# Kernel tuning notes

Hardware: AMD Instinct MI355X
Metric: run time of the kernel (lower is better)

The kernel has to match this reference:

```python
import jax, jax.numpy as jnp
import numpy as np

D = 1024
EXPAND = 2
DI = EXPAND * D
K = 4           # d_conv
C = 64          # chunk_size
ALPHA = 0.9     # memory decay
B, S = 2, 8192
EPS = 1e-5


def setup_inputs() -> dict:
    key = jax.random.key(0)
    ks = jax.random.split(key, 10)
    s = 0.02
    return {
        "x": jax.random.normal(ks[0], (B, S, D), dtype=jnp.float32),
        "norm_w": jnp.ones((D,), dtype=jnp.float32),
        "w_up": jax.random.normal(ks[1], (D, DI), dtype=jnp.float32) * s,
        "w_gate": jax.random.normal(ks[2], (D, DI), dtype=jnp.float32) * s,
        "w_down": jax.random.normal(ks[3], (DI, D), dtype=jnp.float32) * s,
        "conv_w": jax.random.normal(ks[4], (K, 1, DI), dtype=jnp.float32) * s,  # WIO depthwise
        "conv_b": jnp.zeros((DI,), dtype=jnp.float32),
        "wq": jax.random.normal(ks[5], (D, D), dtype=jnp.float32) * s,
        "wk": jax.random.normal(ks[6], (D, D), dtype=jnp.float32) * s,
        "wv": jax.random.normal(ks[7], (D, D), dtype=jnp.float32) * s,
        "wo": jax.random.normal(ks[8], (D, D), dtype=jnp.float32) * s,
    }


def _rmsnorm(x, w):
    ms = jnp.mean(jnp.square(x.astype(jnp.float32)), axis=-1, keepdims=True)
    return (x * jax.lax.rsqrt(ms + EPS).astype(x.dtype)) * w


def _causal_depthwise_conv(u, conv_w, conv_b):
    # u: [B,S,DI]; depthwise causal conv over S, then SiLU
    y = jax.lax.conv_general_dilated(
        u, conv_w,
        window_strides=(1,), padding=[(K - 1, 0)],
        dimension_numbers=("NWC", "WIO", "NWC"),
        feature_group_count=DI)
    return jax.nn.silu(y + conv_b)


def _hebbian_memory(h, wq, wk, wv, wo):
    # chunked linear-attention style Hebbian memory
    b, s, d = h.shape
    n = s // C
    scale = d ** -0.5
    q = (h @ wq).reshape(b, n, C, d) * scale
    k = (h @ wk).reshape(b, n, C, d)
    v = (h @ wv).reshape(b, n, C, d)
    mask = jnp.tril(jnp.ones((C, C), dtype=h.dtype))  # inclusive causal within chunk

    def step(M, qkv):
        qc, kc, vc = qkv  # [b,C,d]
        inter = jnp.einsum("bcd,bde->bce", qc, M)
        attn = jnp.einsum("bcd,bed->bce", qc, kc) * mask
        intra = jnp.einsum("bce,bed->bcd", attn, vc)
        M_new = ALPHA * M + jnp.einsum("bcd,bce->bde", kc, vc)
        return M_new, inter + intra

    M0 = jnp.zeros((b, d, d), dtype=h.dtype)
    qkv = (jnp.swapaxes(q, 0, 1), jnp.swapaxes(k, 0, 1), jnp.swapaxes(v, 0, 1))
    _, o = jax.lax.scan(step, M0, qkv)        # [n,b,C,d]
    o = jnp.swapaxes(o, 0, 1).reshape(b, s, d)
    return o @ wo


def reference(x, norm_w, w_up, w_gate, w_down, conv_w, conv_b, wq, wk, wv, wo):
    normed = _rmsnorm(x, norm_w)
    val = _causal_depthwise_conv(normed @ w_up, conv_w, conv_b)   # [B,S,DI]
    gate = jax.nn.silu(normed @ w_gate)
    out = (gate * val) @ w_down                                   # [B,S,D]
    out = _hebbian_memory(out, wq, wk, wv, wo)
    return x + out
```

## Files before the change

### kernel.cpp

```cpp
#include <hip/hip_runtime.h>
#include <cstdint>
#include <cstddef>

#define SS 8192
#define DD 1024
#define DI2 2048
#define NR 16384

#define LOG2_09 (-0.152003093445050f)
#define LAMBDA16 0.185302018885184f

typedef __attribute__((ext_vector_type(4))) float f32x4;
typedef __attribute__((ext_vector_type(8))) __bf16 bf16x8;

union U16 { uint4 u; bf16x8 b; };

static __device__ __forceinline__ f32x4 MFMA(uint4 a, uint4 b, f32x4 c) {
  U16 ua, ub; ua.u = a; ub.u = b;
  return __builtin_amdgcn_mfma_f32_16x16x32_bf16(ua.b, ub.b, c, 0, 0, 0);
}

static __device__ __forceinline__ unsigned short f2bf(float f) {
  union { float f; unsigned u; } v; v.f = f;
  return (unsigned short)((v.u + 0x7FFFu + ((v.u >> 16) & 1u)) >> 16);
}
static __device__ __forceinline__ float bf2f(unsigned b) {
  union { unsigned u; float f; } v; v.u = b << 16; return v.f;
}
static __device__ __forceinline__ void unpack8(uint4 u, float* f) {
  f[0] = bf2f(u.x & 0xFFFFu); f[1] = bf2f(u.x >> 16);
  f[2] = bf2f(u.y & 0xFFFFu); f[3] = bf2f(u.y >> 16);
  f[4] = bf2f(u.z & 0xFFFFu); f[5] = bf2f(u.z >> 16);
  f[6] = bf2f(u.w & 0xFFFFu); f[7] = bf2f(u.w >> 16);
}
static __device__ __forceinline__ uint4 scale8(uint4 u, float w) {
  float f[8]; unpack8(u, f);
  uint4 o;
  o.x = (unsigned)f2bf(f[0] * w) | ((unsigned)f2bf(f[1] * w) << 16);
  o.y = (unsigned)f2bf(f[2] * w) | ((unsigned)f2bf(f[3] * w) << 16);
  o.z = (unsigned)f2bf(f[4] * w) | ((unsigned)f2bf(f[5] * w) << 16);
  o.w = (unsigned)f2bf(f[6] * w) | ((unsigned)f2bf(f[7] * w) << 16);
  return o;
}

static __device__ __forceinline__ void glds16(const unsigned short* g, char* l) {
  __builtin_amdgcn_global_load_lds(
      (const __attribute__((address_space(1))) unsigned int*)g,
      (__attribute__((address_space(3))) unsigned int*)l, 16, 0, 0);
}

static __device__ __forceinline__ int swz64(int row, int kb) { return ((row << 6) | kb) ^ ((row & 7) << 4); }

__global__ __launch_bounds__(256)
void transpose_cast(const float* __restrict__ in, unsigned short* __restrict__ out, int R, int Cc) {
  __shared__ float tile[32][33];
  const int r0 = blockIdx.y * 32, c0 = blockIdx.x * 32;
  const int tx = threadIdx.x, ty = threadIdx.y;
#pragma unroll
  for (int i = 0; i < 4; i++)
    tile[ty + i * 8][tx] = in[(size_t)(r0 + ty + i * 8) * Cc + c0 + tx];
  __syncthreads();
#pragma unroll
  for (int i = 0; i < 4; i++)
    out[(size_t)(c0 + ty + i * 8) * R + r0 + tx] = f2bf(tile[tx][ty + i * 8]);
}

__global__ __launch_bounds__(256)
void rmsnorm_kernel(const float* __restrict__ x, const float* __restrict__ w,
                    unsigned short* __restrict__ out) {
  const int row = blockIdx.x, t = threadIdx.x;
  const float4 v = ((const float4*)(x + (size_t)row * DD))[t];
  float ss = v.x * v.x + v.y * v.y + v.z * v.z + v.w * v.w;
  __shared__ float sred[256];
  sred[t] = ss;
  __syncthreads();
  for (int o = 128; o > 0; o >>= 1) {
    if (t < o) sred[t] += sred[t + o];
    __syncthreads();
  }
  const float rr = rsqrtf(sred[0] * (1.0f / (float)DD) + 1e-5f);
  const float4 wv = ((const float4*)w)[t];
  uint2 pk;
  pk.x = (unsigned)f2bf(v.x * rr * wv.x) | ((unsigned)f2bf(v.y * rr * wv.y) << 16);
  pk.y = (unsigned)f2bf(v.z * rr * wv.z) | ((unsigned)f2bf(v.w * rr * wv.w) << 16);
  *(uint2*)(out + (size_t)row * DD + t * 4) = pk;
}

enum { EP_BF16 = 0, EP_BF16_BOTH = 1, EP_BF16_T = 2, EP_F32_RES = 3 };

template <int MODE>
__global__ __launch_bounds__(512, 2)
void gemm256(const unsigned short* __restrict__ A, const unsigned short* __restrict__ Bt,
             unsigned short* __restrict__ Cb, unsigned short* __restrict__ Ct,
             float* __restrict__ Cf, const float* __restrict__ resid,
             int M, int N, int K, float scale) {
  __shared__ char sLds[131072];
  const int t = threadIdx.x, lane = t & 63, wid = t >> 6;
  const int wr = wid >> 2, wc = wid & 3;
  const int l15 = lane & 15, lh = lane >> 4;
  const int mblocks = M >> 8;
  const int msl = mblocks >> 3;
  const int xcd = (int)blockIdx.x & 7, loc = (int)blockIdx.x >> 3;
  const int m0 = (xcd * msl + (loc % msl)) << 8;
  const int n0 = (loc / msl) << 8;
  const int srow = wid * 16 + (lane >> 2);
  const int scol = ((lane & 3) << 3) ^ (((srow >> 1) & 3) << 3);
  const unsigned short* pA0 = A + (size_t)(m0 + srow) * K + scol;
  const unsigned short* pA1 = pA0 + (size_t)128 * K;
  const unsigned short* pB0 = Bt + (size_t)(n0 + srow) * K + scol;
  const unsigned short* pB1 = pB0 + (size_t)128 * K;
  const int ldsW = wid * 1024;
  int offA[8], offB[4];
#pragma unroll
  for (int mf = 0; mf < 8; mf++) {
    const int r = wr * 128 + mf * 16 + l15;
    offA[mf] = r * 64 + ((lh * 16) ^ (((r >> 1) & 3) << 4));
  }
#pragma unroll
  for (int nf = 0; nf < 4; nf++) {
    const int r = wc * 64 + nf * 16 + l15;
    offB[nf] = r * 64 + ((lh * 16) ^ (((r >> 1) & 3) << 4));
  }
  const int NT = K >> 5;
#define BUFA(tt) (sLds + ((tt) & 3) * 32768)
#define BUFB(tt) (sLds + ((tt) & 3) * 32768 + 16384)
#define STAGEA(tt) do { const int _k = (tt) * 32; \
    glds16(pA0 + _k, BUFA(tt) + ldsW); \
    glds16(pA1 + _k, BUFA(tt) + 8192 + ldsW); } while (0)
#define STAGEB(tt) do { const int _k = (tt) * 32; \
    glds16(pB0 + _k, BUFB(tt) + ldsW); \
    glds16(pB1 + _k, BUFB(tt) + 8192 + ldsW); } while (0)
  STAGEA(0); STAGEB(0); STAGEA(1); STAGEB(1); STAGEA(2); STAGEB(2);
  asm volatile("s_waitcnt vmcnt(8)" ::: "memory");
  __builtin_amdgcn_s_barrier();
  f32x4 acc[8][4] = {};
  for (int kt = 0; kt < NT; ++kt) {
    const char* At  = BUFA(kt);
    const char* Bt_ = BUFB(kt);
    uint4 av[4], bv[4], av2[4];
#pragma unroll
    for (int i = 0; i < 4; i++) av[i] = *(const uint4*)(At + offA[i]);
#pragma unroll
    for (int i = 0; i < 4; i++) bv[i] = *(const uint4*)(Bt_ + offB[i]);
    if (kt + 3 < NT) STAGEA(kt + 3);
    asm volatile("s_waitcnt lgkmcnt(0)" ::: "memory");
    __builtin_amdgcn_sched_barrier(0);
    __builtin_amdgcn_s_setprio(1);
#pragma unroll
    for (int mf = 0; mf < 4; mf++)
#pragma unroll
      for (int nf = 0; nf < 4; nf++)
        acc[mf][nf] = MFMA(av[mf], bv[nf], acc[mf][nf]);
    __builtin_amdgcn_s_setprio(0);
    __builtin_amdgcn_s_barrier();
#pragma unroll
    for (int i = 0; i < 4; i++) av2[i] = *(const uint4*)(At + offA[4 + i]);
    if (kt + 3 < NT) STAGEB(kt + 3);
    asm volatile("s_waitcnt lgkmcnt(0)" ::: "memory");
    __builtin_amdgcn_sched_barrier(0);
    __builtin_amdgcn_s_setprio(1);
#pragma unroll
    for (int mf = 0; mf < 4; mf++)
#pragma unroll
      for (int nf = 0; nf < 4; nf++)
        acc[4 + mf][nf] = MFMA(av2[mf], bv[nf], acc[4 + mf][nf]);
    __builtin_amdgcn_s_setprio(0);
    if (kt < NT - 3)       { asm volatile("s_waitcnt vmcnt(8)" ::: "memory"); }
    else if (kt == NT - 3) { asm volatile("s_waitcnt vmcnt(4)" ::: "memory"); }
    else if (kt == NT - 2) { asm volatile("s_waitcnt vmcnt(0)" ::: "memory"); }
    __builtin_amdgcn_s_barrier();
  }
#undef STAGEA
#undef STAGEB
#undef BUFA
#undef BUFB
#pragma unroll
  for (int mf = 0; mf < 8; mf++) {
    const int r0 = m0 + wr * 128 + mf * 16 + lh * 4;
#pragma unroll
    for (int nf = 0; nf < 4; nf++) {
      const int c = n0 + wc * 64 + nf * 16 + l15;
      f32x4 v = acc[mf][nf] * scale;
      if constexpr (MODE == EP_F32_RES) {
#pragma unroll
        for (int jj = 0; jj < 4; jj++) {
          const size_t idx = (size_t)(r0 + jj) * N + c;
          Cf[idx] = v[jj] + resid[idx];
        }
      } else {
        if constexpr (MODE == EP_BF16 || MODE == EP_BF16_BOTH) {
#pragma unroll
          for (int jj = 0; jj < 4; jj++)
            Cb[(size_t)(r0 + jj) * N + c] = f2bf(v[jj]);
        }
        if constexpr (MODE == EP_BF16_BOTH || MODE == EP_BF16_T) {
          const int bb = r0 >> 13, s0 = r0 & (SS - 1);
          uint2 pk;
          pk.x = (unsigned)f2bf(v[0]) | ((unsigned)f2bf(v[1]) << 16);
          pk.y = (unsigned)f2bf(v[2]) | ((unsigned)f2bf(v[3]) << 16);
          *(uint2*)(Ct + ((size_t)bb * DD + c) * SS + s0) = pk;
        }
      }
    }
  }
}

__global__ __launch_bounds__(256)
void convgate_kernel(const unsigned short* __restrict__ ug, const float* __restrict__ cw,
                     const float* __restrict__ cb, unsigned short* __restrict__ hin) {
  const int r = blockIdx.x;
  const int c0 = threadIdx.x * 8;
  const int s = r & (SS - 1);
  float acc[8];
#pragma unroll
  for (int i = 0; i < 8; i++) acc[i] = cb[c0 + i];
  for (int tap = 0; tap < 4; tap++) {
    const int ds = s - 3 + tap;
    if (ds < 0) continue;
    uint4 uv = *(const uint4*)(ug + (size_t)(r - 3 + tap) * 4096 + c0);
    float u[8]; unpack8(uv, u);
#pragma unroll
    for (int i = 0; i < 8; i++) acc[i] += u[i] * cw[tap * DI2 + c0 + i];
  }
  uint4 gv = *(const uint4*)(ug + (size_t)r * 4096 + DI2 + c0);
  float gt[8]; unpack8(gv, gt);
  unsigned short o16[8];
#pragma unroll
  for (int i = 0; i < 8; i++) {
    const float val = acc[i] / (1.0f + __expf(-acc[i]));
    const float gg  = gt[i] / (1.0f + __expf(-gt[i]));
    o16[i] = f2bf(val * gg);
  }
  uint4 ov;
  ov.x = (unsigned)o16[0] | ((unsigned)o16[1] << 16);
  ov.y = (unsigned)o16[2] | ((unsigned)o16[3] << 16);
  ov.z = (unsigned)o16[4] | ((unsigned)o16[5] << 16);
  ov.w = (unsigned)o16[6] | ((unsigned)o16[7] << 16);
  *(uint4*)(hin + (size_t)r * DI2 + c0) = ov;
}

__global__ __launch_bounds__(256)
void state_gemm(const unsigned short* __restrict__ vt, const unsigned short* __restrict__ kt,
                unsigned short* __restrict__ Tb) {
  __shared__ char sA[8192];
  __shared__ char sB[8192];
  const int t = threadIdx.x, lane = t & 63, wid = t >> 6;
  const int wr = wid >> 1, wc = wid & 1;
  const int l15 = lane & 15, lh = lane >> 4;
  const int gb = blockIdx.z, b = gb >> 3, g = gb & 7;
  const int m0 = blockIdx.y * 128, n0 = blockIdx.x * 128;
  const int sr = t >> 2, skb = (t & 3) * 16;
  const size_t kofs = (size_t)g * 1024;
  const unsigned short* Ar0 = vt + (size_t)(b * DD + m0 + sr) * SS + kofs;
  const unsigned short* Ar1 = Ar0 + (size_t)64 * SS;
  const unsigned short* Br0 = kt + (size_t)(b * DD + n0 + sr) * SS + kofs;
  const unsigned short* Br1 = Br0 + (size_t)64 * SS;
  f32x4 acc[4][4] = {};
  for (int k0 = 0; k0 < 1024; k0 += 32) {
    const int ke = k0 + (t & 3) * 8;
    const float w = exp2f((float)(15 - (ke >> 6)) * LOG2_09);
    uint4 ra0 = scale8(*(const uint4*)(Ar0 + ke), w);
    uint4 ra1 = scale8(*(const uint4*)(Ar1 + ke), w);
    uint4 rb0 = *(const uint4*)(Br0 + ke);
    uint4 rb1 = *(const uint4*)(Br1 + ke);
    __syncthreads();
    *(uint4*)(sA + swz64(sr, skb)) = ra0;
    *(uint4*)(sA + swz64(sr + 64, skb)) = ra1;
    *(uint4*)(sB + swz64(sr, skb)) = rb0;
    *(uint4*)(sB + swz64(sr + 64, skb)) = rb1;
    __syncthreads();
    uint4 af[4], bfr[4];
#pragma unroll
    for (int i = 0; i < 4; i++) af[i]  = *(uint4*)(sA + swz64(wr * 64 + i * 16 + l15, lh * 16));
#pragma unroll
    for (int i = 0; i < 4; i++) bfr[i] = *(uint4*)(sB + swz64(wc * 64 + i * 16 + l15, lh * 16));
#pragma unroll
    for (int mf = 0; mf < 4; mf++)
#pragma unroll
      for (int nf = 0; nf < 4; nf++)
        acc[mf][nf] = MFMA(af[mf], bfr[nf], acc[mf][nf]);
  }
  unsigned short* Tg = Tb + ((size_t)gb << 20);
#pragma unroll
  for (int mf = 0; mf < 4; mf++) {
    const int r0 = m0 + wr * 64 + mf * 16 + lh * 4;
#pragma unroll
    for (int nf = 0; nf < 4; nf++) {
      const int c = n0 + wc * 64 + nf * 16 + l15;
#pragma unroll
      for (int jj = 0; jj < 4; jj++)
        Tg[(size_t)(r0 + jj) * 1024 + c] = f2bf(acc[mf][nf][jj]);
    }
  }
}

__global__ __launch_bounds__(256)
void prefix_kernel(unsigned short* __restrict__ Tb) {
  const int tid = blockIdx.x * 256 + threadIdx.x;
  const int b = tid >> 17, i = tid & 131071;
  unsigned short* p = Tb + (((size_t)b * 8) << 20) + (size_t)i * 8;
  float acc[8] = {};
  for (int g = 0; g < 8; g++) {
    unsigned short* pg = p + ((size_t)g << 20);
    uint4 tv = *(uint4*)pg;
    float tf_[8]; unpack8(tv, tf_);
    uint4 ov;
    ov.x = (unsigned)f2bf(acc[0]) | ((unsigned)f2bf(acc[1]) << 16);
    ov.y = (unsigned)f2bf(acc[2]) | ((unsigned)f2bf(acc[3]) << 16);
    ov.z = (unsigned)f2bf(acc[4]) | ((unsigned)f2bf(acc[5]) << 16);
    ov.w = (unsigned)f2bf(acc[6]) | ((unsigned)f2bf(acc[7]) << 16);
    *(uint4*)pg = ov;
#pragma unroll
    for (int e = 0; e < 8; e++) acc[e] = LAMBDA16 * acc[e] + tf_[e];
  }
}

__global__ __launch_bounds__(256)
void score_attn(const unsigned short* __restrict__ q, const unsigned short* __restrict__ k,
                unsigned short* __restrict__ sbuf) {
  __shared__ char sQ[4096];
  __shared__ char sK[4096];
  const int p = blockIdx.x, gb = blockIdx.y;
  int qt = (int)((sqrtf(8.0f * p + 1.0f) - 1.0f) * 0.5f);
  while ((qt + 1) * (qt + 2) / 2 <= p) qt++;
  while (qt * (qt + 1) / 2 > p) qt--;
  const int tb = p - qt * (qt + 1) / 2;
  const int b = gb >> 3, g = gb & 7;
  const int t = threadIdx.x, lane = t & 63, wid = t >> 6;
  const int l15 = lane & 15, lh = lane >> 4;
  const int srow = wid * 16 + (lane >> 2), scol = (lane & 3) * 8;
  const unsigned short* qg = q + (size_t)(b * SS + g * 1024 + qt * 64 + srow) * DD + scol;
  const unsigned short* kg = k + (size_t)(b * SS + g * 1024 + tb * 64 + srow) * DD + scol;
  char* lQ = sQ + wid * 1024;
  char* lK = sK + wid * 1024;
  f32x4 s[4] = {};
  for (int k0 = 0; k0 < DD; k0 += 32) {
    glds16(qg + k0, lQ);
    glds16(kg + k0, lK);
    __syncthreads();
    uint4 aq = *(uint4*)(sQ + (wid * 16 + l15) * 64 + lh * 16);
#pragma unroll
    for (int tf = 0; tf < 4; tf++) {
      uint4 bk = *(uint4*)(sK + (tf * 16 + l15) * 64 + lh * 16);
      s[tf] = MFMA(aq, bk, s[tf]);
    }
    __syncthreads();
  }
  const bool diag = (tb == qt);
  const float w = diag ? 1.0f : exp2f((float)(qt - 1 - tb) * LOG2_09);
  unsigned short* sb = sbuf + ((size_t)(gb * 16 + qt) * 64) * 1024 + tb * 64;
#pragma unroll
  for (int tf = 0; tf < 4; tf++)
#pragma unroll
    for (int jj = 0; jj < 4; jj++) {
      const int qr = wid * 16 + lh * 4 + jj;
      const int tc = tf * 16 + l15;
      float val = s[tf][jj] * w;
      if (diag && tc > qr) val = 0.0f;
      sb[(size_t)qr * 1024 + tc] = f2bf(val);
    }
}

__global__ __launch_bounds__(256)
void pv_attn(const unsigned short* __restrict__ sbuf, const unsigned short* __restrict__ vt,
             unsigned short* __restrict__ obuf) {
  __shared__ char sA[4096];
  __shared__ char sB[8192];
  const int et = blockIdx.x, qt = blockIdx.y, gb = blockIdx.z;
  const int b = gb >> 3, g = gb & 7;
  const int t = threadIdx.x, lane = t & 63, wid = t >> 6;
  const int l15 = lane & 15, lh = lane >> 4;
  const int srow = wid * 16 + (lane >> 2), scol = (lane & 3) * 8;
  const int e0 = et * 128;
  const unsigned short* Ag = sbuf + ((size_t)(gb * 16 + qt) * 64 + srow) * 1024 + scol;
  const unsigned short* Bg0 = vt + ((size_t)b * DD + e0 + srow) * SS + g * 1024 + scol;
  const unsigned short* Bg1 = Bg0 + (size_t)64 * SS;
  char* lA  = sA + wid * 1024;
  char* lB0 = sB + wid * 1024;
  char* lB1 = sB + 4096 + wid * 1024;
  const int tEnd = (qt + 1) * 64;
  f32x4 o[4][2] = {};
  for (int t0 = 0; t0 < tEnd; t0 += 32) {
    glds16(Ag + t0, lA);
    glds16(Bg0 + t0, lB0);
    glds16(Bg1 + t0, lB1);
    __syncthreads();
    uint4 af[4], vf[2];
#pragma unroll
    for (int mf = 0; mf < 4; mf++) af[mf] = *(uint4*)(sA + (mf * 16 + l15) * 64 + lh * 16);
#pragma unroll
    for (int nf = 0; nf < 2; nf++) vf[nf] = *(uint4*)(sB + (wid * 32 + nf * 16 + l15) * 64 + lh * 16);
#pragma unroll
    for (int mf = 0; mf < 4; mf++)
#pragma unroll
      for (int nf = 0; nf < 2; nf++)
        o[mf][nf] = MFMA(af[mf], vf[nf], o[mf][nf]);
    __syncthreads();
  }
  const size_t qrow0 = (size_t)b * SS + (size_t)g * 1024 + (size_t)qt * 64;
#pragma unroll
  for (int mf = 0; mf < 4; mf++)
#pragma unroll
    for (int nf = 0; nf < 2; nf++)
#pragma unroll
      for (int jj = 0; jj < 4; jj++)
        obuf[(qrow0 + mf * 16 + lh * 4 + jj) * DD + e0 + wid * 32 + nf * 16 + l15] =
            f2bf(o[mf][nf][jj]);
}

__global__ __launch_bounds__(256)
void cross_gemm(const unsigned short* __restrict__ q, const unsigned short* __restrict__ Minit,
                unsigned short* __restrict__ obuf) {
  __shared__ char sA[8192];
  __shared__ char sB[8192];
  const int t = threadIdx.x, lane = t & 63, wid = t >> 6;
  const int wr = wid >> 1, wc = wid & 1;
  const int l15 = lane & 15, lh = lane >> 4;
  const int gb = blockIdx.z, b = gb >> 3, g = gb & 7;
  const int m0 = blockIdx.y * 128, n0 = blockIdx.x * 128;
  const int srow = wid * 16 + (lane >> 2), scol = (lane & 3) * 8;
  const unsigned short* Ar0 = q + (size_t)(b * SS + g * 1024 + m0 + srow) * DD + scol;
  const unsigned short* Ar1 = Ar0 + (size_t)64 * DD;
  const unsigned short* Br0 = Minit + ((size_t)gb << 20) + (size_t)(n0 + srow) * 1024 + scol;
  const unsigned short* Br1 = Br0 + (size_t)64 * 1024;
  char* lA0 = sA + wid * 1024;
  char* lA1 = sA + 4096 + wid * 1024;
  char* lB0 = sB + wid * 1024;
  char* lB1 = sB + 4096 + wid * 1024;
  f32x4 acc[4][4] = {};
  for (int k0 = 0; k0 < 1024; k0 += 32) {
    glds16(Ar0 + k0, lA0);
    glds16(Ar1 + k0, lA1);
    glds16(Br0 + k0, lB0);
    glds16(Br1 + k0, lB1);
    __syncthreads();
    uint4 af[4], bfr[4];
#pragma unroll
    for (int i = 0; i < 4; i++) af[i]  = *(uint4*)(sA + (wr * 64 + i * 16 + l15) * 64 + lh * 16);
#pragma unroll
    for (int i = 0; i < 4; i++) bfr[i] = *(uint4*)(sB + (wc * 64 + i * 16 + l15) * 64 + lh * 16);
#pragma unroll
    for (int mf = 0; mf < 4; mf++)
#pragma unroll
      for (int nf = 0; nf < 4; nf++)
        acc[mf][nf] = MFMA(af[mf], bfr[nf], acc[mf][nf]);
    __syncthreads();
  }
#pragma unroll
  for (int mf = 0; mf < 4; mf++) {
    const int rl = m0 + wr * 64 + mf * 16 + lh * 4;
#pragma unroll
    for (int nf = 0; nf < 4; nf++) {
      const int c = n0 + wc * 64 + nf * 16 + l15;
#pragma unroll
      for (int jj = 0; jj < 4; jj++) {
        const int r = rl + jj;
        const float rs = exp2f((float)(r >> 6) * LOG2_09);
        const size_t idx = ((size_t)b * SS + (size_t)g * 1024 + r) * DD + c;
        obuf[idx] = f2bf(bf2f(obuf[idx]) + acc[mf][nf][jj] * rs);
      }
    }
  }
}

extern "C" void kernel_launch(void* const* d_in, const int* in_sizes, int n_in,
                              void* d_out, int out_size, void* d_ws, size_t ws_size,
                              hipStream_t stream) {
  (void)in_sizes; (void)n_in; (void)out_size;
  const float* x      = (const float*)d_in[0];
  const float* norm_w = (const float*)d_in[1];
  const float* w_up   = (const float*)d_in[2];
  const float* w_gate = (const float*)d_in[3];
  const float* w_down = (const float*)d_in[4];
  const float* conv_w = (const float*)d_in[5];
  const float* conv_b = (const float*)d_in[6];
  const float* wq     = (const float*)d_in[7];
  const float* wk     = (const float*)d_in[8];
  const float* wv     = (const float*)d_in[9];
  const float* wo     = (const float*)d_in[10];
  float* out = (float*)d_out;

  const size_t MB = 1ull << 20;
  if (ws_size < 212 * MB) return;
  char* base = (char*)d_ws;
  unsigned short* ug     = (unsigned short*)(base + 0);
  unsigned short* hbuf   = (unsigned short*)(base + 0);
  unsigned short* Tbuf   = (unsigned short*)(base + 0);
  unsigned short* qbuf   = (unsigned short*)(base + 32 * MB);
  unsigned short* kbuf   = (unsigned short*)(base + 64 * MB);
  unsigned short* ktbuf  = (unsigned short*)(base + 96 * MB);
  unsigned short* sbuf   = (unsigned short*)(base + 96 * MB);
  unsigned short* normed = (unsigned short*)(base + 128 * MB);
  unsigned short* hin    = (unsigned short*)(base + 128 * MB);
  unsigned short* vtbuf  = (unsigned short*)(base + 128 * MB);
  unsigned short* obuf   = (unsigned short*)(base + 160 * MB);
  unsigned short* wugt   = (unsigned short*)(base + 192 * MB);
  unsigned short* wdt    = (unsigned short*)(base + 200 * MB);
  unsigned short* wqt    = (unsigned short*)(base + 204 * MB);
  unsigned short* wkt    = (unsigned short*)(base + 206 * MB);
  unsigned short* wvt    = (unsigned short*)(base + 208 * MB);
  unsigned short* wot    = (unsigned short*)(base + 210 * MB);

  dim3 tb(32, 8);
  transpose_cast<<<dim3(DI2 / 32, DD / 32), tb, 0, stream>>>(w_up,   wugt,                    DD,  DI2);
  transpose_cast<<<dim3(DI2 / 32, DD / 32), tb, 0, stream>>>(w_gate, wugt + (size_t)DI2 * DD, DD,  DI2);
  transpose_cast<<<dim3(DD / 32, DI2 / 32), tb, 0, stream>>>(w_down, wdt, DI2, DD);
  transpose_cast<<<dim3(DD / 32, DD / 32),  tb, 0, stream>>>(wq, wqt, DD, DD);
  transpose_cast<<<dim3(DD / 32, DD / 32),  tb, 0, stream>>>(wk, wkt, DD, DD);
  transpose_cast<<<dim3(DD / 32, DD / 32),  tb, 0, stream>>>(wv, wvt, DD, DD);
  transpose_cast<<<dim3(DD / 32, DD / 32),  tb, 0, stream>>>(wo, wot, DD, DD);

  rmsnorm_kernel<<<NR, 256, 0, stream>>>(x, norm_w, normed);

  gemm256<EP_BF16><<<dim3((NR / 256) * (4096 / 256)), 512, 0, stream>>>(
      normed, wugt, ug, nullptr, nullptr, nullptr, NR, 4096, DD, 1.0f);

  convgate_kernel<<<NR, 256, 0, stream>>>(ug, conv_w, conv_b, hin);

  gemm256<EP_BF16><<<dim3((NR / 256) * (DD / 256)), 512, 0, stream>>>(
      hin, wdt, hbuf, nullptr, nullptr, nullptr, NR, DD, DI2, 1.0f);

  gemm256<EP_BF16><<<dim3((NR / 256) * (DD / 256)), 512, 0, stream>>>(
      hbuf, wqt, qbuf, nullptr, nullptr, nullptr, NR, DD, DD, 0.03125f);
  gemm256<EP_BF16_BOTH><<<dim3((NR / 256) * (DD / 256)), 512, 0, stream>>>(
      hbuf, wkt, kbuf, ktbuf, nullptr, nullptr, NR, DD, DD, 1.0f);
  gemm256<EP_BF16_T><<<dim3((NR / 256) * (DD / 256)), 512, 0, stream>>>(
      hbuf, wvt, nullptr, vtbuf, nullptr, nullptr, NR, DD, DD, 1.0f);

  state_gemm<<<dim3(8, 8, 16), 256, 0, stream>>>(vtbuf, ktbuf, Tbuf);
  score_attn<<<dim3(136, 16), 256, 0, stream>>>(qbuf, kbuf, sbuf);
  prefix_kernel<<<1024, 256, 0, stream>>>(Tbuf);
  pv_attn<<<dim3(8, 16, 16), 256, 0, stream>>>(sbuf, vtbuf, obuf);
  cross_gemm<<<dim3(8, 8, 16), 256, 0, stream>>>(qbuf, Tbuf, obuf);

  gemm256<EP_F32_RES><<<dim3((NR / 256) * (DD / 256)), 512, 0, stream>>>(
      obuf, wot, nullptr, nullptr, out, x, NR, DD, DD, 1.0f);
}
```

Measured before the change: 760.5 us.

## Route state and cross GEMMs through the pipelined 256-tile GEMM kernel

Removes the separate state_gemm and cross_gemm kernels and runs both through the gemm256 template with new epilogue modes, added lda/ldb strides and batched z-dimension offsets. The decay weighting that state_gemm applied to V on the fly moves into the K-transpose epilogue of the K projection GEMM. The 128x128 single-buffered tiles are replaced by the 256x256 four-stage global-to-LDS pipeline. Extra s_barrier calls are inserted after each staging step in the main loop, which adds synchronisation to every GEMM, and each state/cross launch now has only 256 blocks.

```diff
diff --git a/kernel.cpp b/kernel.cpp
--- a/kernel.cpp
+++ b/kernel.cpp
@@ -33,23 +33,12 @@
   f[4] = bf2f(u.z & 0xFFFFu); f[5] = bf2f(u.z >> 16);
   f[6] = bf2f(u.w & 0xFFFFu); f[7] = bf2f(u.w >> 16);
 }
-static __device__ __forceinline__ uint4 scale8(uint4 u, float w) {
-  float f[8]; unpack8(u, f);
-  uint4 o;
-  o.x = (unsigned)f2bf(f[0] * w) | ((unsigned)f2bf(f[1] * w) << 16);
-  o.y = (unsigned)f2bf(f[2] * w) | ((unsigned)f2bf(f[3] * w) << 16);
-  o.z = (unsigned)f2bf(f[4] * w) | ((unsigned)f2bf(f[5] * w) << 16);
-  o.w = (unsigned)f2bf(f[6] * w) | ((unsigned)f2bf(f[7] * w) << 16);
-  return o;
-}
 
 static __device__ __forceinline__ void glds16(const unsigned short* g, char* l) {
   __builtin_amdgcn_global_load_lds(
       (const __attribute__((address_space(1))) unsigned int*)g,
       (__attribute__((address_space(3))) unsigned int*)l, 16, 0, 0);
 }
-
-static __device__ __forceinline__ int swz64(int row, int kb) { return ((row << 6) | kb) ^ ((row & 7) << 4); }
 
 __global__ __launch_bounds__(256)
 void transpose_cast(const float* __restrict__ in, unsigned short* __restrict__ out, int R, int Cc) {
@@ -86,29 +75,49 @@
   *(uint2*)(out + (size_t)row * DD + t * 4) = pk;
 }
 
-enum { EP_BF16 = 0, EP_BF16_BOTH = 1, EP_BF16_T = 2, EP_F32_RES = 3 };
+enum { EP_BF16 = 0, EP_BF16_BOTH = 1, EP_BF16_T = 2, EP_F32_RES = 3, EP_STATE = 4, EP_CROSS = 5 };
 
 template <int MODE>
 __global__ __launch_bounds__(512, 2)
 void gemm256(const unsigned short* __restrict__ A, const unsigned short* __restrict__ Bt,
              unsigned short* __restrict__ Cb, unsigned short* __restrict__ Ct,
              float* __restrict__ Cf, const float* __restrict__ resid,
-             int M, int N, int K, float scale) {
+             int M, int N, int kLen, int lda, int ldb, float scale) {
   __shared__ char sLds[131072];
   const int t = threadIdx.x, lane = t & 63, wid = t >> 6;
   const int wr = wid >> 2, wc = wid & 3;
   const int l15 = lane & 15, lh = lane >> 4;
   const int mblocks = M >> 8;
-  const int msl = mblocks >> 3;
-  const int xcd = (int)blockIdx.x & 7, loc = (int)blockIdx.x >> 3;
-  const int m0 = (xcd * msl + (loc % msl)) << 8;
-  const int n0 = (loc / msl) << 8;
+  int m0, n0;
+  if ((mblocks & 7) == 0) {
+    const int msl = mblocks >> 3;
+    const int xcd = (int)blockIdx.x & 7, loc = (int)blockIdx.x >> 3;
+    m0 = (xcd * msl + (loc % msl)) << 8;
+    n0 = (loc / msl) << 8;
+  } else {
+    m0 = ((int)blockIdx.x % mblocks) << 8;
+    n0 = ((int)blockIdx.x / mblocks) << 8;
+  }
+  int zb = 0, zg = 0;
+  const unsigned short* Abase = A;
+  const unsigned short* Bbase = Bt;
+  if constexpr (MODE == EP_STATE || MODE == EP_CROSS) {
+    const int gb = blockIdx.z;
+    zb = gb >> 3; zg = gb & 7;
+    if constexpr (MODE == EP_STATE) {
+      Abase = A + (size_t)zb * DD * SS + (size_t)zg * 1024;
+      Bbase = Bt + (size_t)zb * DD * SS + (size_t)zg * 1024;
+    } else {
+      Abase = A + ((size_t)zb * SS + (size_t)zg * 1024) * (size_t)lda;
+      Bbase = Bt + ((size_t)blockIdx.z << 20);
+    }
+  }
   const int srow = wid * 16 + (lane >> 2);
   const int scol = ((lane & 3) << 3) ^ (((srow >> 1) & 3) << 3);
-  const unsigned short* pA0 = A + (size_t)(m0 + srow) * K + scol;
-  const unsigned short* pA1 = pA0 + (size_t)128 * K;
-  const unsigned short* pB0 = Bt + (size_t)(n0 + srow) * K + scol;
-  const unsigned short* pB1 = pB0 + (size_t)128 * K;
+  const unsigned short* pA0 = Abase + (size_t)(m0 + srow) * lda + scol;
+  const unsigned short* pA1 = pA0 + (size_t)128 * lda;
+  const unsigned short* pB0 = Bbase + (size_t)(n0 + srow) * ldb + scol;
+  const unsigned short* pB1 = pB0 + (size_t)128 * ldb;
   const int ldsW = wid * 1024;
   int offA[8], offB[4];
 #pragma unroll
@@ -121,7 +130,7 @@
     const int r = wc * 64 + nf * 16 + l15;
     offB[nf] = r * 64 + ((lh * 16) ^ (((r >> 1) & 3) << 4));
   }
-  const int NT = K >> 5;
+  const int NT = kLen >> 5;
 #define BUFA(tt) (sLds + ((tt) & 3) * 32768)
 #define BUFB(tt) (sLds + ((tt) & 3) * 32768 + 16384)
 #define STAGEA(tt) do { const int _k = (tt) * 32; \
@@ -143,6 +152,7 @@
 #pragma unroll
     for (int i = 0; i < 4; i++) bv[i] = *(const uint4*)(Bt_ + offB[i]);
     if (kt + 3 < NT) STAGEA(kt + 3);
+    __builtin_amdgcn_s_barrier();
     asm volatile("s_waitcnt lgkmcnt(0)" ::: "memory");
     __builtin_amdgcn_sched_barrier(0);
     __builtin_amdgcn_s_setprio(1);
@@ -156,6 +166,7 @@
 #pragma unroll
     for (int i = 0; i < 4; i++) av2[i] = *(const uint4*)(At + offA[4 + i]);
     if (kt + 3 < NT) STAGEB(kt + 3);
+    __builtin_amdgcn_s_barrier();
     asm volatile("s_waitcnt lgkmcnt(0)" ::: "memory");
     __builtin_amdgcn_sched_barrier(0);
     __builtin_amdgcn_s_setprio(1);
@@ -187,6 +198,18 @@
           const size_t idx = (size_t)(r0 + jj) * N + c;
           Cf[idx] = v[jj] + resid[idx];
         }
+      } else if constexpr (MODE == EP_STATE) {
+        unsigned short* Tg = Cb + ((size_t)blockIdx.z << 20);
+#pragma unroll
+        for (int jj = 0; jj < 4; jj++)
+          Tg[(size_t)(r0 + jj) * 1024 + c] = f2bf(v[jj]);
+      } else if constexpr (MODE == EP_CROSS) {
+        const float rs = exp2f((float)(r0 >> 6) * LOG2_09);
+#pragma unroll
+        for (int jj = 0; jj < 4; jj++) {
+          const size_t idx = ((size_t)zb * SS + (size_t)zg * 1024 + r0 + jj) * DD + c;
+          Cb[idx] = f2bf(bf2f(Cb[idx]) + v[jj] * rs);
+        }
       } else {
         if constexpr (MODE == EP_BF16 || MODE == EP_BF16_BOTH) {
 #pragma unroll
@@ -195,9 +218,12 @@
         }
         if constexpr (MODE == EP_BF16_BOTH || MODE == EP_BF16_T) {
           const int bb = r0 >> 13, s0 = r0 & (SS - 1);
+          float wt = 1.0f;
+          if constexpr (MODE == EP_BF16_BOTH)
+            wt = exp2f((float)(15 - ((s0 >> 6) & 15)) * LOG2_09);
           uint2 pk;
-          pk.x = (unsigned)f2bf(v[0]) | ((unsigned)f2bf(v[1]) << 16);
-          pk.y = (unsigned)f2bf(v[2]) | ((unsigned)f2bf(v[3]) << 16);
+          pk.x = (unsigned)f2bf(v[0] * wt) | ((unsigned)f2bf(v[1] * wt) << 16);
+          pk.y = (unsigned)f2bf(v[2] * wt) | ((unsigned)f2bf(v[3] * wt) << 16);
           *(uint2*)(Ct + ((size_t)bb * DD + c) * SS + s0) = pk;
         }
       }
@@ -237,61 +263,6 @@
   ov.z = (unsigned)o16[4] | ((unsigned)o16[5] << 16);
   ov.w = (unsigned)o16[6] | ((unsigned)o16[7] << 16);
   *(uint4*)(hin + (size_t)r * DI2 + c0) = ov;
-}
-
-__global__ __launch_bounds__(256)
-void state_gemm(const unsigned short* __restrict__ vt, const unsigned short* __restrict__ kt,
-                unsigned short* __restrict__ Tb) {
-  __shared__ char sA[8192];
-  __shared__ char sB[8192];
-  const int t = threadIdx.x, lane = t & 63, wid = t >> 6;
-  const int wr = wid >> 1, wc = wid & 1;
-  const int l15 = lane & 15, lh = lane >> 4;
-  const int gb = blockIdx.z, b = gb >> 3, g = gb & 7;
-  const int m0 = blockIdx.y * 128, n0 = blockIdx.x * 128;
-  const int sr = t >> 2, skb = (t & 3) * 16;
-  const size_t kofs = (size_t)g * 1024;
-  const unsigned short* Ar0 = vt + (size_t)(b * DD + m0 + sr) * SS + kofs;
-  const unsigned short* Ar1 = Ar0 + (size_t)64 * SS;
-  const unsigned short* Br0 = kt + (size_t)(b * DD + n0 + sr) * SS + kofs;
-  const unsigned short* Br1 = Br0 + (size_t)64 * SS;
-  f32x4 acc[4][4] = {};
-  for (int k0 = 0; k0 < 1024; k0 += 32) {
-    const int ke = k0 + (t & 3) * 8;
-    const float w = exp2f((float)(15 - (ke >> 6)) * LOG2_09);
-    uint4 ra0 = scale8(*(const uint4*)(Ar0 + ke), w);
-    uint4 ra1 = scale8(*(const uint4*)(Ar1 + ke), w);
-    uint4 rb0 = *(const uint4*)(Br0 + ke);
-    uint4 rb1 = *(const uint4*)(Br1 + ke);
-    __syncthreads();
-    *(uint4*)(sA + swz64(sr, skb)) = ra0;
-    *(uint4*)(sA + swz64(sr + 64, skb)) = ra1;
-    *(uint4*)(sB + swz64(sr, skb)) = rb0;
-    *(uint4*)(sB + swz64(sr + 64, skb)) = rb1;
-    __syncthreads();
-    uint4 af[4], bfr[4];
-#pragma unroll
-    for (int i = 0; i < 4; i++) af[i]  = *(uint4*)(sA + swz64(wr * 64 + i * 16 + l15, lh * 16));
-#pragma unroll
-    for (int i = 0; i < 4; i++) bfr[i] = *(uint4*)(sB + swz64(wc * 64 + i * 16 + l15, lh * 16));
-#pragma unroll
-    for (int mf = 0; mf < 4; mf++)
-#pragma unroll
-      for (int nf = 0; nf < 4; nf++)
-        acc[mf][nf] = MFMA(af[mf], bfr[nf], acc[mf][nf]);
-  }
-  unsigned short* Tg = Tb + ((size_t)gb << 20);
-#pragma unroll
-  for (int mf = 0; mf < 4; mf++) {
-    const int r0 = m0 + wr * 64 + mf * 16 + lh * 4;
-#pragma unroll
-    for (int nf = 0; nf < 4; nf++) {
-      const int c = n0 + wc * 64 + nf * 16 + l15;
-#pragma unroll
-      for (int jj = 0; jj < 4; jj++)
-        Tg[(size_t)(r0 + jj) * 1024 + c] = f2bf(acc[mf][nf][jj]);
-    }
-  }
 }
 
 __global__ __launch_bounds__(256)
@@ -408,61 +379,6 @@
             f2bf(o[mf][nf][jj]);
 }
 
-__global__ __launch_bounds__(256)
-void cross_gemm(const unsigned short* __restrict__ q, const unsigned short* __restrict__ Minit,
-                unsigned short* __restrict__ obuf) {
-  __shared__ char sA[8192];
-  __shared__ char sB[8192];
-  const int t = threadIdx.x, lane = t & 63, wid = t >> 6;
-  const int wr = wid >> 1, wc = wid & 1;
-  const int l15 = lane & 15, lh = lane >> 4;
-  const int gb = blockIdx.z, b = gb >> 3, g = gb & 7;
-  const int m0 = blockIdx.y * 128, n0 = blockIdx.x * 128;
-  const int srow = wid * 16 + (lane >> 2), scol = (lane & 3) * 8;
-  const unsigned short* Ar0 = q + (size_t)(b * SS + g * 1024 + m0 + srow) * DD + scol;
-  const unsigned short* Ar1 = Ar0 + (size_t)64 * DD;
-  const unsigned short* Br0 = Minit + ((size_t)gb << 20) + (size_t)(n0 + srow) * 1024 + scol;
-  const unsigned short* Br1 = Br0 + (size_t)64 * 1024;
-  char* lA0 = sA + wid * 1024;
-  char* lA1 = sA + 4096 + wid * 1024;
-  char* lB0 = sB + wid * 1024;
-  char* lB1 = sB + 4096 + wid * 1024;
-  f32x4 acc[4][4] = {};
-  for (int k0 = 0; k0 < 1024; k0 += 32) {
-    glds16(Ar0 + k0, lA0);
-    glds16(Ar1 + k0, lA1);
-    glds16(Br0 + k0, lB0);
-    glds16(Br1 + k0, lB1);
-    __syncthreads();
-    uint4 af[4], bfr[4];
-#pragma unroll
-    for (int i = 0; i < 4; i++) af[i]  = *(uint4*)(sA + (wr * 64 + i * 16 + l15) * 64 + lh * 16);
-#pragma unroll
-    for (int i = 0; i < 4; i++) bfr[i] = *(uint4*)(sB + (wc * 64 + i * 16 + l15) * 64 + lh * 16);
-#pragma unroll
-    for (int mf = 0; mf < 4; mf++)
-#pragma unroll
-      for (int nf = 0; nf < 4; nf++)
-        acc[mf][nf] = MFMA(af[mf], bfr[nf], acc[mf][nf]);
-    __syncthreads();
-  }
-#pragma unroll
-  for (int mf = 0; mf < 4; mf++) {
-    const int rl = m0 + wr * 64 + mf * 16 + lh * 4;
-#pragma unroll
-    for (int nf = 0; nf < 4; nf++) {
-      const int c = n0 + wc * 64 + nf * 16 + l15;
-#pragma unroll
-      for (int jj = 0; jj < 4; jj++) {
-        const int r = rl + jj;
-        const float rs = exp2f((float)(r >> 6) * LOG2_09);
-        const size_t idx = ((size_t)b * SS + (size_t)g * 1024 + r) * DD + c;
-        obuf[idx] = f2bf(bf2f(obuf[idx]) + acc[mf][nf][jj] * rs);
-      }
-    }
-  }
-}
-
 extern "C" void kernel_launch(void* const* d_in, const int* in_sizes, int n_in,
                               void* d_out, int out_size, void* d_ws, size_t ws_size,
                               hipStream_t stream) {
@@ -513,26 +429,28 @@
   rmsnorm_kernel<<<NR, 256, 0, stream>>>(x, norm_w, normed);
 
   gemm256<EP_BF16><<<dim3((NR / 256) * (4096 / 256)), 512, 0, stream>>>(
-      normed, wugt, ug, nullptr, nullptr, nullptr, NR, 4096, DD, 1.0f);
+      normed, wugt, ug, nullptr, nullptr, nullptr, NR, 4096, DD, DD, DD, 1.0f);
 
   convgate_kernel<<<NR, 256, 0, stream>>>(ug, conv_w, conv_b, hin);
 
   gemm256<EP_BF16><<<dim3((NR / 256) * (DD / 256)), 512, 0, stream>>>(
-      hin, wdt, hbuf, nullptr, nullptr, nullptr, NR, DD, DI2, 1.0f);
+      hin, wdt, hbuf, nullptr, nullptr, nullptr, NR, DD, DI2, DI2, DI2, 1.0f);
 
   gemm256<EP_BF16><<<dim3((NR / 256) * (DD / 256)), 512, 0, stream>>>(
-      hbuf, wqt, qbuf, nullptr, nullptr, nullptr, NR, DD, DD, 0.03125f);
+      hbuf, wqt, qbuf, nullptr, nullptr, nullptr, NR, DD, DD, DD, DD, 0.03125f);
   gemm256<EP_BF16_BOTH><<<dim3((NR / 256) * (DD / 256)), 512, 0, stream>>>(
-      hbuf, wkt, kbuf, ktbuf, nullptr, nullptr, NR, DD, DD, 1.0f);
+      hbuf, wkt, kbuf, ktbuf, nullptr, nullptr, NR, DD, DD, DD, DD, 1.0f);
   gemm256<EP_BF16_T><<<dim3((NR / 256) * (DD / 256)), 512, 0, stream>>>(
-      hbuf, wvt, nullptr, vtbuf, nullptr, nullptr, NR, DD, DD, 1.0f);
-
-  state_gemm<<<dim3(8, 8, 16), 256, 0, stream>>>(vtbuf, ktbuf, Tbuf);
+      hbuf, wvt, nullptr, vtbuf, nullptr, nullptr, NR, DD, DD, DD, DD, 1.0f);
+
+  gemm256<EP_STATE><<<dim3(16, 1, 16), 512, 0, stream>>>(
+      vtbuf, ktbuf, Tbuf, nullptr, nullptr, nullptr, 1024, 1024, 1024, SS, SS, 1.0f);
   score_attn<<<dim3(136, 16), 256, 0, stream>>>(qbuf, kbuf, sbuf);
   prefix_kernel<<<1024, 256, 0, stream>>>(Tbuf);
   pv_attn<<<dim3(8, 16, 16), 256, 0, stream>>>(sbuf, vtbuf, obuf);
-  cross_gemm<<<dim3(8, 8, 16), 256, 0, stream>>>(qbuf, Tbuf, obuf);
+  gemm256<EP_CROSS><<<dim3(16, 1, 16), 512, 0, stream>>>(
+      qbuf, Tbuf, obuf, nullptr, nullptr, nullptr, 1024, 1024, 1024, DD, 1024, 1.0f);
 
   gemm256<EP_F32_RES><<<dim3((NR / 256) * (DD / 256)), 512, 0, stream>>>(
-      obuf, wot, nullptr, nullptr, out, x, NR, DD, DD, 1.0f);
-}
+      obuf, wot, nullptr, nullptr, out, x, NR, DD, DD, DD, DD, 1.0f);
+}
```

Measured after the change: 743.0 us. 2.3% less time.
